# Performance work log

Measured on AMD Instinct MI355X. Metric: run time of the kernel, lower is better.

Reference implementation:

```python
import jax, jax.numpy as jnp
import numpy as np

N, F_IN, H, OUT, E = 32000, 256, 4, 64, 512000
NEG_SLOPE = 0.2


def setup_inputs() -> dict:
    key = jax.random.key(0)
    ks = jax.random.split(key, 7)
    return {
        "feat": jax.random.normal(ks[0], (N, F_IN), dtype=jnp.float32),
        "dist": jax.random.uniform(ks[1], (E, 1, 1), dtype=jnp.float32),
        "W": jax.random.normal(ks[2], (F_IN, H * OUT), dtype=jnp.float32) * (1.0 / np.sqrt(F_IN)),
        "w_att_src": jax.random.normal(ks[3], (1, H, OUT), dtype=jnp.float32) * 0.1,
        "w_att_dst": jax.random.normal(ks[4], (1, H, OUT), dtype=jnp.float32) * 0.1,
        "src": jax.random.randint(ks[5], (E,), 0, N, dtype=jnp.int32),
        "dst": jax.random.randint(ks[6], (E,), 0, N, dtype=jnp.int32),
    }


def reference(feat, dist, W, w_att_src, w_att_dst, src, dst):
    n = feat.shape[0]
    # dense projection (no bias, no activation) then split heads: [N, H, OUT]
    ft = (feat @ W).reshape(n, H, OUT)
    # per-node attention logits: [N, H, 1]
    e_src = jnp.sum(ft * w_att_src, axis=-1, keepdims=True)
    e_dst = jnp.sum(ft * w_att_dst, axis=-1, keepdims=True)
    # edge logits via u_add_v gather: [E, H, 1]
    e = e_src[src] + e_dst[dst]
    e = jnp.where(e >= 0, e, NEG_SLOPE * e)  # leaky relu
    # edge softmax normalized over incoming edges of each dst node
    emax = jax.ops.segment_max(e, dst, num_segments=n)          # [N, H, 1]
    ex = jnp.exp(e - emax[dst])
    denom = jax.ops.segment_sum(ex, dst, num_segments=n)        # [N, H, 1]
    a = (ex / denom[dst]) * dist                                # [E, H, 1]
    # message = u_mul_e, aggregate = sum over incoming edges
    m = ft[src] * a                                             # [E, H, OUT]
    out = jax.ops.segment_sum(m, dst, num_segments=n)           # [N, H, OUT]
    return out.reshape(n, H * OUT)
```

## Files before the change

kernel.cpp:

```cpp
#include <hip/hip_runtime.h>

#define F_IN 256
#define NHEAD 4
#define DOUT 64
#define FOUT 256
#define NEG_SLOPE 0.2f
#define BCAP 64
#define PREP_BLKS 16

typedef __attribute__((ext_vector_type(8))) short bf16x8;
typedef __attribute__((ext_vector_type(4))) float f32x4;

__device__ __forceinline__ unsigned short f2bf(float x) {
    unsigned u = __float_as_uint(x);
    return (unsigned short)((u + 0x7FFFu + ((u >> 16) & 1u)) >> 16);
}
__device__ __forceinline__ float bflo(unsigned u) { return __uint_as_float(u << 16); }
__device__ __forceinline__ float bfhi(unsigned u) { return __uint_as_float(u & 0xFFFF0000u); }

__global__ __launch_bounds__(256) void k_prep_zero(
    const float* __restrict__ W, unsigned short* __restrict__ Wt,
    int* __restrict__ cnt, int n)
{
    if (blockIdx.x < PREP_BLKS) {
        __shared__ float tile[64][65];
        int bi = blockIdx.x >> 2, bj = blockIdx.x & 3;
        int t = threadIdx.x;
        int r0 = t >> 6, c = t & 63;
#pragma unroll
        for (int it = 0; it < 16; ++it) {
            int r = it * 4 + r0;
            tile[r][c] = W[(size_t)(bi * 64 + r) * FOUT + bj * 64 + c];
        }
        __syncthreads();
#pragma unroll
        for (int it = 0; it < 16; ++it) {
            int r = it * 4 + r0;
            Wt[(size_t)(bj * 64 + r) * F_IN + bi * 64 + c] = f2bf(tile[c][r]);
        }
        return;
    }
    int i = (blockIdx.x - PREP_BLKS) * 256 + threadIdx.x;
    if (i < n / 4) ((int4*)cnt)[i] = make_int4(0, 0, 0, 0);
}

__global__ __launch_bounds__(256) void k_gemm_fill(
    const float* __restrict__ feat, const unsigned short* __restrict__ Wt,
    const float* __restrict__ wsrc, const float* __restrict__ wdst,
    unsigned short* __restrict__ ftb, float* __restrict__ esrc,
    float* __restrict__ edst,
    const int* __restrict__ src, const int* __restrict__ dst,
    const float* __restrict__ dist, int* __restrict__ cnt,
    int2* __restrict__ bkt, int E_, int GB)
{
    if (blockIdx.x >= GB) {
        int e = (blockIdx.x - GB) * 256 + threadIdx.x;
        if (e >= E_) return;
        int d = dst[e];
        int p = atomicAdd(&cnt[d], 1);
        if (p < BCAP) bkt[(size_t)d * BCAP + p] = make_int2(src[e], __float_as_int(dist[e]));
        return;
    }

    __shared__ unsigned short A_lds[64 * 40];
    const int m0   = blockIdx.x * 64;
    const int tid  = threadIdx.x;
    const int w    = tid >> 6;
    const int lane = tid & 63;
    const int l15  = lane & 15, l4 = lane >> 4;

    const int srow = tid >> 2, skg = tid & 3;
    const float* gA = &feat[(size_t)(m0 + srow) * F_IN + skg * 8];
    unsigned short* sA = &A_lds[srow * 40 + skg * 8];

    f32x4 acc[4][4];
#pragma unroll
    for (int mi = 0; mi < 4; ++mi)
#pragma unroll
        for (int ni = 0; ni < 4; ++ni)
            acc[mi][ni] = (f32x4){0.f, 0.f, 0.f, 0.f};

    for (int ks = 0; ks < F_IN / 32; ++ks) {
        float4 a0 = *(const float4*)(gA + ks * 32);
        float4 a1 = *(const float4*)(gA + ks * 32 + 4);
        if (ks) __syncthreads();
        bf16x8 pk;
        pk[0] = (short)f2bf(a0.x); pk[1] = (short)f2bf(a0.y);
        pk[2] = (short)f2bf(a0.z); pk[3] = (short)f2bf(a0.w);
        pk[4] = (short)f2bf(a1.x); pk[5] = (short)f2bf(a1.y);
        pk[6] = (short)f2bf(a1.z); pk[7] = (short)f2bf(a1.w);
        *(bf16x8*)sA = pk;
        __syncthreads();

        bf16x8 bfr[4];
#pragma unroll
        for (int ni = 0; ni < 4; ++ni)
            bfr[ni] = *(const bf16x8*)&Wt[(size_t)(w * 64 + ni * 16 + l15) * F_IN + ks * 32 + l4 * 8];
        bf16x8 afr[4];
#pragma unroll
        for (int mi = 0; mi < 4; ++mi)
            afr[mi] = *(const bf16x8*)&A_lds[(mi * 16 + l15) * 40 + l4 * 8];
#pragma unroll
        for (int mi = 0; mi < 4; ++mi)
#pragma unroll
            for (int ni = 0; ni < 4; ++ni)
                acc[mi][ni] = __builtin_amdgcn_mfma_f32_16x16x32_bf16(
                    afr[mi], bfr[ni], acc[mi][ni], 0, 0, 0);
    }

    float wsv[4], wdv[4];
#pragma unroll
    for (int ni = 0; ni < 4; ++ni) {
        wsv[ni] = wsrc[w * 64 + ni * 16 + l15];
        wdv[ni] = wdst[w * 64 + ni * 16 + l15];
    }
#pragma unroll
    for (int mi = 0; mi < 4; ++mi) {
#pragma unroll
        for (int r = 0; r < 4; ++r) {
            int row = m0 + mi * 16 + l4 * 4 + r;
            float ps = 0.f, pd = 0.f;
#pragma unroll
            for (int ni = 0; ni < 4; ++ni) {
                float v = acc[mi][ni][r];
                ftb[(size_t)row * FOUT + w * 64 + ni * 16 + l15] = f2bf(v);
                ps += v * wsv[ni];
                pd += v * wdv[ni];
            }
#pragma unroll
            for (int m = 1; m < 16; m <<= 1) {
                ps += __shfl_xor(ps, m);
                pd += __shfl_xor(pd, m);
            }
            if (l15 == 0) {
                esrc[row * NHEAD + w] = ps;
                edst[row * NHEAD + w] = pd;
            }
        }
    }
}

__global__ __launch_bounds__(256) void k_agg(
    const int* __restrict__ cnt, const int2* __restrict__ bkt,
    const float* __restrict__ esrc, const float* __restrict__ edst,
    const unsigned short* __restrict__ ftb, float* __restrict__ out, int n)
{
    int node = blockIdx.x * 4 + (threadIdx.x >> 6);
    if (node >= n) return;
    int lane = threadIdx.x & 63;
    int half = lane >> 5;
    int col  = (lane & 31) * 8;
    int h    = (lane & 31) >> 3;
    int cn = cnt[node]; if (cn > BCAP) cn = BCAP;
    const int2* b = &bkt[(size_t)node * BCAP];
    float ed = edst[node * NHEAD + h];

    float denom = 0.f;
    float acc[8] = {0,0,0,0,0,0,0,0};

    for (int i = 0; i < cn; i += 4) {
        int jA = i + half, jB = i + 2 + half;
        bool vA = jA < cn, vB = jB < cn;
        int2 cA = make_int2(0, 0), cB = make_int2(0, 0);
        if (vA) cA = b[jA];
        if (vB) cB = b[jB];

        float lgA = esrc[cA.x * NHEAD + h] + ed;
        float lgB = esrc[cB.x * NHEAD + h] + ed;
        lgA = (lgA >= 0.f) ? lgA : NEG_SLOPE * lgA;
        lgB = (lgB >= 0.f) ? lgB : NEG_SLOPE * lgB;
        float pA = vA ? __expf(lgA) : 0.f;
        float pB = vB ? __expf(lgB) : 0.f;

        int4 rA = *(const int4*)&ftb[(size_t)cA.x * FOUT + col];
        int4 rB = *(const int4*)&ftb[(size_t)cB.x * FOUT + col];

        float aA = pA * __int_as_float(cA.y);
        float aB = pB * __int_as_float(cB.y);
        denom += pA + pB;

        acc[0] += bflo(rA.x) * aA + bflo(rB.x) * aB;
        acc[1] += bfhi(rA.x) * aA + bfhi(rB.x) * aB;
        acc[2] += bflo(rA.y) * aA + bflo(rB.y) * aB;
        acc[3] += bfhi(rA.y) * aA + bfhi(rB.y) * aB;
        acc[4] += bflo(rA.z) * aA + bflo(rB.z) * aB;
        acc[5] += bfhi(rA.z) * aA + bfhi(rB.z) * aB;
        acc[6] += bflo(rA.w) * aA + bflo(rB.w) * aB;
        acc[7] += bfhi(rA.w) * aA + bfhi(rB.w) * aB;
    }

    denom += __shfl_xor(denom, 32);
#pragma unroll
    for (int k = 0; k < 8; ++k) acc[k] += __shfl_xor(acc[k], 32);

    float inv = (denom > 0.f) ? 1.f / denom : 0.f;
    if (half == 0) {
        float4 o0 = { acc[0] * inv, acc[1] * inv, acc[2] * inv, acc[3] * inv };
        float4 o1 = { acc[4] * inv, acc[5] * inv, acc[6] * inv, acc[7] * inv };
        *(float4*)&out[(size_t)node * FOUT + col]     = o0;
        *(float4*)&out[(size_t)node * FOUT + col + 4] = o1;
    }
}

extern "C" void kernel_launch(void* const* d_in, const int* in_sizes, int n_in,
                              void* d_out, int out_size, void* d_ws, size_t ws_size,
                              hipStream_t stream)
{
    const float* feat = (const float*)d_in[0];
    const float* dist = (const float*)d_in[1];
    const float* W    = (const float*)d_in[2];
    const float* wsrc = (const float*)d_in[3];
    const float* wdst = (const float*)d_in[4];
    const int*   src  = (const int*)d_in[5];
    const int*   dst  = (const int*)d_in[6];
    float* out = (float*)d_out;

    const int n  = in_sizes[0] / F_IN;
    const int E_ = in_sizes[5];

    float* ws = (float*)d_ws;
    size_t off = 0;
    unsigned short* ftb = (unsigned short*)(ws + off); off += (size_t)n * FOUT / 2;
    unsigned short* Wt  = (unsigned short*)(ws + off); off += (size_t)F_IN * FOUT / 2;
    float* esrc = ws + off; off += (size_t)n * NHEAD;
    float* edst = ws + off; off += (size_t)n * NHEAD;
    int2*  bkt  = (int2*)(ws + off); off += (size_t)n * BCAP * 2;
    int*   cnt  = (int*)(ws + off);  off += (size_t)n;

    const int ZB = (n / 4 + 255) / 256;
    k_prep_zero<<<PREP_BLKS + ZB, 256, 0, stream>>>(W, Wt, cnt, n);

    const int GB = n / 64;
    const int FB = (E_ + 255) / 256;
    k_gemm_fill<<<GB + FB, 256, 0, stream>>>(feat, Wt, wsrc, wdst, ftb, esrc, edst,
                                             src, dst, dist, cnt, bkt, E_, GB);

    k_agg<<<(n + 3) / 4, 256, 0, stream>>>(cnt, bkt, esrc, edst, ftb, out, n);
}
```

Measured before the change: 84.38 us.

## Quantize projected features to int8 with per-head scale for aggregation gathers

Stores the projected node features as int8 with a per-row-per-head absmax scale instead of bf16, packing the scale alongside the source logit in one int2. The gathered row then takes 256 bytes instead of 512. The aggregation kernel is reorganised so each lane decodes 16 int8 values and four edge groups are processed per step, with a reduction across the groups at the end. The GEMM epilogue stages the quantized tile in LDS so it can be written out with coalesced stores. This trades gather bandwidth for lower precision, which could breach the accuracy tolerance.

Result: faster. 70.49 us (-16.5%).

```diff
diff --git a/kernel.cpp b/kernel.cpp
--- a/kernel.cpp
+++ b/kernel.cpp
@@ -7,6 +7,7 @@
 #define NEG_SLOPE 0.2f
 #define BCAP 64
 #define PREP_BLKS 16
+#define QSTRIDE 272
 
 typedef __attribute__((ext_vector_type(8))) short bf16x8;
 typedef __attribute__((ext_vector_type(4))) float f32x4;
@@ -15,8 +16,6 @@
     unsigned u = __float_as_uint(x);
     return (unsigned short)((u + 0x7FFFu + ((u >> 16) & 1u)) >> 16);
 }
-__device__ __forceinline__ float bflo(unsigned u) { return __uint_as_float(u << 16); }
-__device__ __forceinline__ float bfhi(unsigned u) { return __uint_as_float(u & 0xFFFF0000u); }
 
 __global__ __launch_bounds__(256) void k_prep_zero(
     const float* __restrict__ W, unsigned short* __restrict__ Wt,
@@ -47,7 +46,7 @@
 __global__ __launch_bounds__(256) void k_gemm_fill(
     const float* __restrict__ feat, const unsigned short* __restrict__ Wt,
     const float* __restrict__ wsrc, const float* __restrict__ wdst,
-    unsigned short* __restrict__ ftb, float* __restrict__ esrc,
+    signed char* __restrict__ qft, int2* __restrict__ pk,
     float* __restrict__ edst,
     const int* __restrict__ src, const int* __restrict__ dst,
     const float* __restrict__ dist, int* __restrict__ cnt,
@@ -63,6 +62,7 @@
     }
 
     __shared__ unsigned short A_lds[64 * 40];
+    __shared__ signed char q_lds[64 * QSTRIDE];
     const int m0   = blockIdx.x * 64;
     const int tid  = threadIdx.x;
     const int w    = tid >> 6;
@@ -84,12 +84,12 @@
         float4 a0 = *(const float4*)(gA + ks * 32);
         float4 a1 = *(const float4*)(gA + ks * 32 + 4);
         if (ks) __syncthreads();
-        bf16x8 pk;
-        pk[0] = (short)f2bf(a0.x); pk[1] = (short)f2bf(a0.y);
-        pk[2] = (short)f2bf(a0.z); pk[3] = (short)f2bf(a0.w);
-        pk[4] = (short)f2bf(a1.x); pk[5] = (short)f2bf(a1.y);
-        pk[6] = (short)f2bf(a1.z); pk[7] = (short)f2bf(a1.w);
-        *(bf16x8*)sA = pk;
+        bf16x8 pkv;
+        pkv[0] = (short)f2bf(a0.x); pkv[1] = (short)f2bf(a0.y);
+        pkv[2] = (short)f2bf(a0.z); pkv[3] = (short)f2bf(a0.w);
+        pkv[4] = (short)f2bf(a1.x); pkv[5] = (short)f2bf(a1.y);
+        pkv[6] = (short)f2bf(a1.z); pkv[7] = (short)f2bf(a1.w);
+        *(bf16x8*)sA = pkv;
         __syncthreads();
 
         bf16x8 bfr[4];
@@ -119,86 +119,111 @@
 #pragma unroll
         for (int r = 0; r < 4; ++r) {
             int row = m0 + mi * 16 + l4 * 4 + r;
-            float ps = 0.f, pd = 0.f;
+            float ps = 0.f, pd = 0.f, mx = 0.f;
 #pragma unroll
             for (int ni = 0; ni < 4; ++ni) {
                 float v = acc[mi][ni][r];
-                ftb[(size_t)row * FOUT + w * 64 + ni * 16 + l15] = f2bf(v);
                 ps += v * wsv[ni];
                 pd += v * wdv[ni];
+                mx = fmaxf(mx, fabsf(v));
             }
 #pragma unroll
             for (int m = 1; m < 16; m <<= 1) {
                 ps += __shfl_xor(ps, m);
                 pd += __shfl_xor(pd, m);
+                mx = fmaxf(mx, __shfl_xor(mx, m));
+            }
+            float inv_s = 127.0f / fmaxf(mx, 1e-20f);
+#pragma unroll
+            for (int ni = 0; ni < 4; ++ni) {
+                int q = __float2int_rn(acc[mi][ni][r] * inv_s);
+                q = (q > 127) ? 127 : ((q < -127) ? -127 : q);
+                q_lds[(mi * 16 + l4 * 4 + r) * QSTRIDE + w * 64 + ni * 16 + l15] = (signed char)q;
             }
             if (l15 == 0) {
-                esrc[row * NHEAD + w] = ps;
+                pk[row * NHEAD + w] = make_int2(__float_as_int(ps),
+                                                __float_as_int(mx * (1.0f / 127.0f)));
                 edst[row * NHEAD + w] = pd;
             }
         }
+    }
+    __syncthreads();
+    {
+        int row = tid >> 2, seg = tid & 3;
+        const int4* s = (const int4*)&q_lds[row * QSTRIDE + seg * 64];
+        int4* d4 = (int4*)&qft[(size_t)(m0 + row) * FOUT + seg * 64];
+        d4[0] = s[0]; d4[1] = s[1]; d4[2] = s[2]; d4[3] = s[3];
     }
 }
 
 __global__ __launch_bounds__(256) void k_agg(
     const int* __restrict__ cnt, const int2* __restrict__ bkt,
-    const float* __restrict__ esrc, const float* __restrict__ edst,
-    const unsigned short* __restrict__ ftb, float* __restrict__ out, int n)
+    const int2* __restrict__ pk, const float* __restrict__ edst,
+    const signed char* __restrict__ qft, float* __restrict__ out, int n)
 {
     int node = blockIdx.x * 4 + (threadIdx.x >> 6);
     if (node >= n) return;
     int lane = threadIdx.x & 63;
-    int half = lane >> 5;
-    int col  = (lane & 31) * 8;
-    int h    = (lane & 31) >> 3;
+    int g = lane >> 4;
+    int l = lane & 15;
+    int h = l >> 2;
     int cn = cnt[node]; if (cn > BCAP) cn = BCAP;
     const int2* b = &bkt[(size_t)node * BCAP];
     float ed = edst[node * NHEAD + h];
 
     float denom = 0.f;
-    float acc[8] = {0,0,0,0,0,0,0,0};
-
-    for (int i = 0; i < cn; i += 4) {
-        int jA = i + half, jB = i + 2 + half;
+    float acc[16];
+#pragma unroll
+    for (int k = 0; k < 16; ++k) acc[k] = 0.f;
+
+    for (int i = 0; i < cn; i += 8) {
+        int jA = i + g, jB = i + 4 + g;
         bool vA = jA < cn, vB = jB < cn;
-        int2 cA = make_int2(0, 0), cB = make_int2(0, 0);
-        if (vA) cA = b[jA];
-        if (vB) cB = b[jB];
-
-        float lgA = esrc[cA.x * NHEAD + h] + ed;
-        float lgB = esrc[cB.x * NHEAD + h] + ed;
+        int2 cA = vA ? b[jA] : make_int2(0, 0);
+        int2 cB = vB ? b[jB] : make_int2(0, 0);
+
+        int4 rA = *(const int4*)&qft[(size_t)cA.x * FOUT + l * 16];
+        int4 rB = *(const int4*)&qft[(size_t)cB.x * FOUT + l * 16];
+        int2 pA2 = pk[cA.x * NHEAD + h];
+        int2 pB2 = pk[cB.x * NHEAD + h];
+
+        float lgA = __int_as_float(pA2.x) + ed;
+        float lgB = __int_as_float(pB2.x) + ed;
         lgA = (lgA >= 0.f) ? lgA : NEG_SLOPE * lgA;
         lgB = (lgB >= 0.f) ? lgB : NEG_SLOPE * lgB;
         float pA = vA ? __expf(lgA) : 0.f;
         float pB = vB ? __expf(lgB) : 0.f;
-
-        int4 rA = *(const int4*)&ftb[(size_t)cA.x * FOUT + col];
-        int4 rB = *(const int4*)&ftb[(size_t)cB.x * FOUT + col];
-
-        float aA = pA * __int_as_float(cA.y);
-        float aB = pB * __int_as_float(cB.y);
         denom += pA + pB;
 
-        acc[0] += bflo(rA.x) * aA + bflo(rB.x) * aB;
-        acc[1] += bfhi(rA.x) * aA + bfhi(rB.x) * aB;
-        acc[2] += bflo(rA.y) * aA + bflo(rB.y) * aB;
-        acc[3] += bfhi(rA.y) * aA + bfhi(rB.y) * aB;
-        acc[4] += bflo(rA.z) * aA + bflo(rB.z) * aB;
-        acc[5] += bfhi(rA.z) * aA + bfhi(rB.z) * aB;
-        acc[6] += bflo(rA.w) * aA + bflo(rB.w) * aB;
-        acc[7] += bfhi(rA.w) * aA + bfhi(rB.w) * aB;
-    }
-
-    denom += __shfl_xor(denom, 32);
-#pragma unroll
-    for (int k = 0; k < 8; ++k) acc[k] += __shfl_xor(acc[k], 32);
+        float aA = pA * __int_as_float(cA.y) * __int_as_float(pA2.y);
+        float aB = pB * __int_as_float(cB.y) * __int_as_float(pB2.y);
+
+        const unsigned wA[4] = {(unsigned)rA.x, (unsigned)rA.y, (unsigned)rA.z, (unsigned)rA.w};
+        const unsigned wB[4] = {(unsigned)rB.x, (unsigned)rB.y, (unsigned)rB.z, (unsigned)rB.w};
+#pragma unroll
+        for (int wd = 0; wd < 4; ++wd) {
+            acc[wd * 4 + 0] += (float)(signed char)(wA[wd])       * aA + (float)(signed char)(wB[wd])       * aB;
+            acc[wd * 4 + 1] += (float)(signed char)(wA[wd] >> 8)  * aA + (float)(signed char)(wB[wd] >> 8)  * aB;
+            acc[wd * 4 + 2] += (float)(signed char)(wA[wd] >> 16) * aA + (float)(signed char)(wB[wd] >> 16) * aB;
+            acc[wd * 4 + 3] += (float)(signed char)(wA[wd] >> 24) * aA + (float)(signed char)(wB[wd] >> 24) * aB;
+        }
+    }
+
+#pragma unroll
+    for (int m = 16; m < 64; m <<= 1) {
+        denom += __shfl_xor(denom, m);
+#pragma unroll
+        for (int k = 0; k < 16; ++k) acc[k] += __shfl_xor(acc[k], m);
+    }
 
     float inv = (denom > 0.f) ? 1.f / denom : 0.f;
-    if (half == 0) {
-        float4 o0 = { acc[0] * inv, acc[1] * inv, acc[2] * inv, acc[3] * inv };
-        float4 o1 = { acc[4] * inv, acc[5] * inv, acc[6] * inv, acc[7] * inv };
-        *(float4*)&out[(size_t)node * FOUT + col]     = o0;
-        *(float4*)&out[(size_t)node * FOUT + col + 4] = o1;
+    if (g == 0) {
+#pragma unroll
+        for (int q4 = 0; q4 < 4; ++q4) {
+            float4 o = { acc[q4 * 4 + 0] * inv, acc[q4 * 4 + 1] * inv,
+                         acc[q4 * 4 + 2] * inv, acc[q4 * 4 + 3] * inv };
+            *(float4*)&out[(size_t)node * FOUT + l * 16 + q4 * 4] = o;
+        }
     }
 }
 
@@ -220,9 +245,9 @@
 
     float* ws = (float*)d_ws;
     size_t off = 0;
-    unsigned short* ftb = (unsigned short*)(ws + off); off += (size_t)n * FOUT / 2;
-    unsigned short* Wt  = (unsigned short*)(ws + off); off += (size_t)F_IN * FOUT / 2;
-    float* esrc = ws + off; off += (size_t)n * NHEAD;
+    signed char* qft = (signed char*)(ws + off); off += (size_t)n * FOUT / 4;
+    unsigned short* Wt = (unsigned short*)(ws + off); off += (size_t)F_IN * FOUT / 2;
+    int2*  pk   = (int2*)(ws + off); off += (size_t)n * NHEAD * 2;
     float* edst = ws + off; off += (size_t)n * NHEAD;
     int2*  bkt  = (int2*)(ws + off); off += (size_t)n * BCAP * 2;
     int*   cnt  = (int*)(ws + off);  off += (size_t)n;
@@ -232,8 +257,8 @@
 
     const int GB = n / 64;
     const int FB = (E_ + 255) / 256;
-    k_gemm_fill<<<GB + FB, 256, 0, stream>>>(feat, Wt, wsrc, wdst, ftb, esrc, edst,
+    k_gemm_fill<<<GB + FB, 256, 0, stream>>>(feat, Wt, wsrc, wdst, qft, pk, edst,
                                              src, dst, dist, cnt, bkt, E_, GB);
 
-    k_agg<<<(n + 3) / 4, 256, 0, stream>>>(cnt, bkt, esrc, edst, ftb, out, n);
-}
+    k_agg<<<(n + 3) / 4, 256, 0, stream>>>(cnt, bkt, pk, edst, qft, out, n);
+}
```
